# Kernel tuning notes

Hardware: AMD Instinct MI355X
Metric: run time of the kernel (lower is better)

## Reference

```python
import jax, jax.numpy as jnp
import numpy as np

NUM_EXPERTS = 16
TOP_K = 2
D_IN = 1024
D_HID = 4096
D_OUT = 1024
BATCH = 8192


def setup_inputs() -> dict:
    key = jax.random.key(0)
    ks = jax.random.split(key, 6)
    s_in = 1.0 / np.sqrt(D_IN)
    s_hid = 1.0 / np.sqrt(D_HID)
    return {
        "x": jax.random.normal(ks[0], (BATCH, D_IN), dtype=jnp.float32),
        "Wg": jax.random.normal(ks[1], (D_IN, NUM_EXPERTS), dtype=jnp.float32) * s_in,
        "W1": jax.random.normal(ks[2], (NUM_EXPERTS, D_IN, D_HID), dtype=jnp.float32) * s_in,
        "b1": jnp.zeros((NUM_EXPERTS, D_HID), dtype=jnp.float32),
        "W2": jax.random.normal(ks[3], (NUM_EXPERTS, D_HID, D_OUT), dtype=jnp.float32) * s_hid,
        "b2": jnp.zeros((NUM_EXPERTS, D_OUT), dtype=jnp.float32),
    }


def _moe_forward(x, Wg, W1, b1, W2, b2):
    # Gating: top-k routing with softmax over the selected logits.
    logits = x @ Wg                                   # [B, E]
    top_vals, top_idx = jax.lax.top_k(logits, TOP_K)  # [B, k]
    routing_weights = jax.nn.softmax(top_vals, axis=-1)  # [B, k]

    # Per-token combine weight for each expert (sum over k slots):
    # cw[b, e] = sum_k routing_weights[b, k] * (top_idx[b, k] == e)
    one_hot = jax.nn.one_hot(top_idx, NUM_EXPERTS, dtype=x.dtype)  # [B, k, E]
    combine_w = jnp.einsum("bk,bke->be", routing_weights, one_hot)  # [B, E]

    # Per-expert MLP compute + weighted scatter-add combine.
    # Fixed-size loop over experts (structurally distinct weight slices);
    # equivalent math to the original's gather/compute/scatter dispatch.
    out = jnp.zeros((x.shape[0], D_OUT), dtype=x.dtype)
    for e in range(NUM_EXPERTS):
        h = jax.nn.relu(x @ W1[e] + b1[e])            # [B, H]
        y = h @ W2[e] + b2[e]                         # [B, O]
        out = out + combine_w[:, e:e + 1] * y
    return out


def reference(x, Wg, W1, b1, W2, b2):
    return _moe_forward(x, Wg, W1, b1, W2, b2)
```

## Files before the change

kernel.cpp:

```cpp
#include <hip/hip_runtime.h>
#include <cstdio>

#define DIN   1024
#define DHID  4096
#define DOUT  1024
#define NEXP  16
#define NTOK  8192
#define NPAIR (NTOK * 2)
#define PADMAX 20480
#define MAXTILES 80

typedef _Float16 h8 __attribute__((ext_vector_type(8)));
typedef _Float16 h4 __attribute__((ext_vector_type(4)));
typedef float    f4 __attribute__((ext_vector_type(4)));

#define C_CNT  0
#define C_POFF 16
#define C_CUR  32
#define C_NT   48
#define C_TE   64
#define C_TP   256

__device__ __forceinline__ void async16(const void* g, void* l) {
  __builtin_amdgcn_global_load_lds((const __attribute__((address_space(1))) void*)g,
                                   (__attribute__((address_space(3))) void*)l, 16, 0, 0);
}

__global__ void k_init(float* __restrict__ out, const float* __restrict__ x,
                       _Float16* __restrict__ x16, int* __restrict__ ptok,
                       float* __restrict__ pw, int* __restrict__ ctrl) {
  int i = blockIdx.x * 256 + threadIdx.x;
  ((f4*)out)[i] = (f4){0.f, 0.f, 0.f, 0.f};
  float4 v = ((const float4*)x)[i];
  h4 hv = {(_Float16)v.x, (_Float16)v.y, (_Float16)v.z, (_Float16)v.w};
  ((h4*)x16)[i] = hv;
  if (i < PADMAX) { ptok[i] = 0; pw[i] = 0.f; }
  if (i < 1024) ctrl[i] = 0;
}

__global__ void k_gate(const float* __restrict__ x, const float* __restrict__ wg,
                       int* __restrict__ te, float* __restrict__ tw,
                       int* __restrict__ ctrl) {
  int t = blockIdx.x * 4 + (threadIdx.x >> 6);
  int l = threadIdx.x & 63;
  const float* xr = x + (long)t * DIN;
  float acc[NEXP];
#pragma unroll
  for (int e = 0; e < NEXP; ++e) acc[e] = 0.f;
  for (int k = l; k < DIN; k += 64) {
    float xv = xr[k];
    const float4* wr = (const float4*)(wg + (long)k * NEXP);
    float4 a = wr[0], b = wr[1], c = wr[2], d = wr[3];
    acc[0]  += xv * a.x; acc[1]  += xv * a.y; acc[2]  += xv * a.z; acc[3]  += xv * a.w;
    acc[4]  += xv * b.x; acc[5]  += xv * b.y; acc[6]  += xv * b.z; acc[7]  += xv * b.w;
    acc[8]  += xv * c.x; acc[9]  += xv * c.y; acc[10] += xv * c.z; acc[11] += xv * c.w;
    acc[12] += xv * d.x; acc[13] += xv * d.y; acc[14] += xv * d.z; acc[15] += xv * d.w;
  }
#pragma unroll
  for (int off = 32; off > 0; off >>= 1) {
#pragma unroll
    for (int e = 0; e < NEXP; ++e) acc[e] += __shfl_xor(acc[e], off, 64);
  }
  if (l == 0) {
    float v0 = -1e30f; int e0 = 0;
#pragma unroll
    for (int e = 0; e < NEXP; ++e) if (acc[e] > v0) { v0 = acc[e]; e0 = e; }
    float v1 = -1e30f; int e1 = 0;
#pragma unroll
    for (int e = 0; e < NEXP; ++e) if (e != e0 && acc[e] > v1) { v1 = acc[e]; e1 = e; }
    float d = expf(v1 - v0);
    float den = 1.f / (1.f + d);
    te[2 * t] = e0;     tw[2 * t] = den;
    te[2 * t + 1] = e1; tw[2 * t + 1] = d * den;
    atomicAdd(&ctrl[C_CNT + e0], 1);
    atomicAdd(&ctrl[C_CNT + e1], 1);
  }
}

__global__ void k_scan(int* __restrict__ ctrl) {
  __shared__ int sOff[NEXP], sT0[NEXP], sTiles[NEXP];
  int tid = threadIdx.x;
  if (tid == 0) {
    int off = 0, nt = 0;
    for (int e = 0; e < NEXP; ++e) {
      int c = ctrl[C_CNT + e];
      int tiles = (c + 255) >> 8;
      ctrl[C_POFF + e] = off;
      ctrl[C_CUR + e] = off;
      sOff[e] = off; sT0[e] = nt; sTiles[e] = tiles;
      nt += tiles;
      off += tiles * 256;
    }
    ctrl[C_NT] = nt;
  }
  __syncthreads();
  int nt = sT0[NEXP - 1] + sTiles[NEXP - 1];
  for (int j = tid; j < nt; j += blockDim.x) {
    int e = 0;
#pragma unroll
    for (int k = 1; k < NEXP; ++k) if (j >= sT0[k]) e = k;
    ctrl[C_TE + j] = e;
    ctrl[C_TP + j] = sOff[e] + (j - sT0[e]) * 256;
  }
}

__global__ void k_assign(const int* __restrict__ te, const float* __restrict__ tw,
                         int* __restrict__ ctrl, int* __restrict__ ptok,
                         float* __restrict__ pw) {
  int t = blockIdx.x * 256 + threadIdx.x;
#pragma unroll
  for (int s = 0; s < 2; ++s) {
    int e = te[2 * t + s];
    int pos = atomicAdd(&ctrl[C_CUR + e], 1);
    ptok[pos] = t;
    pw[pos] = tw[2 * t + s];
  }
}

__global__ void k_transpose(const float* __restrict__ W, _Float16* __restrict__ out,
                            int R, int C) {
  __shared__ __align__(16) _Float16 lds[64 * 128];
  int e = blockIdx.z;
  const float* Wb = W + ((long)e * R + blockIdx.x * 128) * C + blockIdx.y * 64;
  _Float16* ob = out + ((long)e * C + blockIdx.y * 64) * R + blockIdx.x * 128;
  int tid = threadIdx.x;
  int l = tid & 63, w = tid >> 6;
  int c0 = (l & 15) * 4;
  int rq0 = (l >> 4) * 4 + w * 16;
#pragma unroll
  for (int rr = 0; rr < 2; ++rr) {
    int rq = rq0 + rr * 64;
    float4 v0 = *(const float4*)(Wb + (long)(rq + 0) * C + c0);
    float4 v1 = *(const float4*)(Wb + (long)(rq + 1) * C + c0);
    float4 v2 = *(const float4*)(Wb + (long)(rq + 2) * C + c0);
    float4 v3 = *(const float4*)(Wb + (long)(rq + 3) * C + c0);
    int rchunk = rq >> 3, rsub = rq & 7;
    {
      int c = c0 + 0;
      h4 hv = {(_Float16)v0.x, (_Float16)v1.x, (_Float16)v2.x, (_Float16)v3.x};
      *(h4*)&lds[c * 128 + ((rchunk ^ (c & 15)) << 3) + rsub] = hv;
    }
    {
      int c = c0 + 1;
      h4 hv = {(_Float16)v0.y, (_Float16)v1.y, (_Float16)v2.y, (_Float16)v3.y};
      *(h4*)&lds[c * 128 + ((rchunk ^ (c & 15)) << 3) + rsub] = hv;
    }
    {
      int c = c0 + 2;
      h4 hv = {(_Float16)v0.z, (_Float16)v1.z, (_Float16)v2.z, (_Float16)v3.z};
      *(h4*)&lds[c * 128 + ((rchunk ^ (c & 15)) << 3) + rsub] = hv;
    }
    {
      int c = c0 + 3;
      h4 hv = {(_Float16)v0.w, (_Float16)v1.w, (_Float16)v2.w, (_Float16)v3.w};
      *(h4*)&lds[c * 128 + ((rchunk ^ (c & 15)) << 3) + rsub] = hv;
    }
  }
  __syncthreads();
#pragma unroll
  for (int it = 0; it < 4; ++it) {
    int idx = it * 256 + tid;
    int c = idx >> 4, ch = idx & 15;
    h8 v = *(const h8*)&lds[c * 128 + ((ch ^ (c & 15)) << 3)];
    *(h8*)(ob + (long)c * R + ch * 8) = v;
  }
}

template<int KD, int ND, int G1>
__global__ __launch_bounds__(512, 2)
void k_gemm(const _Float16* __restrict__ A, const _Float16* __restrict__ Wt,
            const float* __restrict__ bias, const int* __restrict__ ctrl,
            const int* __restrict__ ptok, const float* __restrict__ pw,
            _Float16* __restrict__ Hout, float* __restrict__ out) {
  __shared__ __align__(16) _Float16 sm[65536];

  constexpr int NB = ND / 256;
  constexpr int NW = NB * MAXTILES;
  constexpr int QX = NW / 8;
  int bid = blockIdx.x;
  int wid = (bid & 7) * QX + (bid >> 3);
  int nb = wid % NB;
  int mt = wid / NB;

  if (mt >= ctrl[C_NT]) return;
  int e  = ctrl[C_TE + mt];
  int p0 = ctrl[C_TP + mt];
  int n0 = nb * 256;
  int tid = threadIdx.x;
  int w = tid >> 6, l = tid & 63;
  int wm = w & 1, wn = w >> 1;
  int ln15 = l & 15, lq = l >> 4;

  const _Float16* agp[4];
  const _Float16* bgp[4];
#pragma unroll
  for (int h = 0; h < 2; ++h)
#pragma unroll
    for (int j = 0; j < 2; ++j) {
      int r = (w * 2 + j) * 8 + (l >> 3);
      int c = (l & 7) ^ (r & 7);
      long arow = G1 ? (long)ptok[p0 + h * 128 + r] : (long)(p0 + h * 128 + r);
      agp[h * 2 + j] = A + arow * KD + c * 8;
      bgp[h * 2 + j] = Wt + ((long)e * ND + n0 + h * 128 + r) * KD + c * 8;
    }

  auto stageH = [&](int t, int half) {
    _Float16* dst = sm + (t & 1) * 32768 + (half & 1) * 16384 + (half >> 1) * 8192
                    + w * 1024;
    long koff = (long)t * 64;
    const _Float16* const* gp = (half & 1) ? bgp : agp;
#pragma unroll
    for (int j = 0; j < 2; ++j)
      async16(gp[(half >> 1) * 2 + j] + koff, dst + j * 512);
  };

  f4 acc[2][4][2][2];
#pragma unroll
  for (int mq = 0; mq < 2; ++mq)
#pragma unroll
    for (int i = 0; i < 4; ++i)
#pragma unroll
      for (int nq = 0; nq < 2; ++nq)
#pragma unroll
        for (int j = 0; j < 2; ++j) acc[mq][i][nq][j] = (f4){0.f, 0.f, 0.f, 0.f};

  h8 af[8], bf0[4], bf1[4];

  auto readA = [&](int d, int mq) {
    const _Float16* Ab = sm + d * 32768 + mq * 8192;
#pragma unroll
    for (int i = 0; i < 4; ++i) {
      int rh = wm * 64 + i * 16 + ln15;
#pragma unroll
      for (int ks = 0; ks < 2; ++ks)
        af[i * 2 + ks] = *(const h8*)&Ab[rh * 64 + (((ks * 4 + lq)) ^ (rh & 7)) * 8];
    }
  };
  auto readB = [&](int d, int nq, h8* bf) {
    const _Float16* Bb = sm + d * 32768 + 16384 + nq * 8192;
#pragma unroll
    for (int j = 0; j < 2; ++j) {
      int rh = wn * 32 + j * 16 + ln15;
#pragma unroll
      for (int ks = 0; ks < 2; ++ks)
        bf[j * 2 + ks] = *(const h8*)&Bb[rh * 64 + (((ks * 4 + lq)) ^ (rh & 7)) * 8];
    }
  };
  auto mfmaQ = [&](int mq, int nq, const h8* bf) {
    __builtin_amdgcn_s_setprio(1);
#pragma unroll
    for (int ks = 0; ks < 2; ++ks)
#pragma unroll
      for (int i = 0; i < 4; ++i)
#pragma unroll
        for (int j = 0; j < 2; ++j)
          acc[mq][i][nq][j] = __builtin_amdgcn_mfma_f32_16x16x32_f16(
              af[i * 2 + ks], bf[j * 2 + ks], acc[mq][i][nq][j], 0, 0, 0);
    __builtin_amdgcn_s_setprio(0);
  };

  constexpr int KSTEPS = KD / 64;

  stageH(0, 0); stageH(0, 1); stageH(0, 2); stageH(0, 3);
  stageH(1, 0); stageH(1, 1); stageH(1, 2);
  asm volatile("s_waitcnt vmcnt(6)" ::: "memory");
  __builtin_amdgcn_s_barrier();

#pragma unroll 2
  for (int t = 0; t < KSTEPS; ++t) {
    int d = t & 1;
    readA(d, 0);
    readB(d, 0, bf0);
    if (t + 1 < KSTEPS) stageH(t + 1, 3);
    __builtin_amdgcn_s_barrier();
    asm volatile("s_waitcnt lgkmcnt(0)" ::: "memory");
    mfmaQ(0, 0, bf0);
    __builtin_amdgcn_s_barrier();
    readB(d, 1, bf1);
    if (t + 2 < KSTEPS) stageH(t + 2, 0);
    __builtin_amdgcn_s_barrier();
    asm volatile("s_waitcnt lgkmcnt(0)" ::: "memory");
    mfmaQ(0, 1, bf1);
    __builtin_amdgcn_s_barrier();
    readA(d, 1);
    if (t + 2 < KSTEPS) stageH(t + 2, 1);
    __builtin_amdgcn_s_barrier();
    asm volatile("s_waitcnt lgkmcnt(0)" ::: "memory");
    mfmaQ(1, 1, bf1);
    __builtin_amdgcn_s_barrier();
    if (t + 2 < KSTEPS) stageH(t + 2, 2);
    if (t + 1 < KSTEPS) {
      if (t + 2 < KSTEPS) asm volatile("s_waitcnt vmcnt(6)" ::: "memory");
      else                asm volatile("s_waitcnt vmcnt(0)" ::: "memory");
    }
    __builtin_amdgcn_s_barrier();
    mfmaQ(1, 0, bf0);
    __builtin_amdgcn_s_barrier();
  }

  float bj[2][2];
#pragma unroll
  for (int nq = 0; nq < 2; ++nq)
#pragma unroll
    for (int j = 0; j < 2; ++j)
      bj[nq][j] = bias[e * ND + n0 + nq * 128 + wn * 32 + j * 16 + ln15];

  if (G1) {
    _Float16* cs = sm;
#pragma unroll
    for (int mq = 0; mq < 2; ++mq) {
      if (mq) __syncthreads();
#pragma unroll
      for (int i = 0; i < 4; ++i)
#pragma unroll
        for (int reg = 0; reg < 4; ++reg) {
          int row = wm * 64 + i * 16 + lq * 4 + reg;
#pragma unroll
          for (int nq = 0; nq < 2; ++nq)
#pragma unroll
            for (int j = 0; j < 2; ++j)
              cs[row * 264 + nq * 128 + wn * 32 + j * 16 + ln15] =
                  (_Float16)fmaxf(acc[mq][i][nq][j][reg] + bj[nq][j], 0.f);
        }
      __syncthreads();
#pragma unroll
      for (int p = 0; p < 8; ++p) {
        int idx = p * 512 + tid;
        int row = idx >> 5, ch = idx & 31;
        *(h8*)(Hout + (long)(p0 + mq * 128 + row) * DHID + n0 + ch * 8) =
            *(const h8*)&cs[row * 264 + ch * 8];
      }
    }
  } else {
#pragma unroll
    for (int mq = 0; mq < 2; ++mq)
#pragma unroll
      for (int i = 0; i < 4; ++i)
#pragma unroll
        for (int reg = 0; reg < 4; ++reg) {
          int p = p0 + mq * 128 + wm * 64 + i * 16 + lq * 4 + reg;
          float wgt = pw[p];
          if (wgt != 0.f) {
            int tk = ptok[p];
            float* orow = out + (long)tk * DOUT + n0;
#pragma unroll
            for (int nq = 0; nq < 2; ++nq)
#pragma unroll
              for (int j = 0; j < 2; ++j)
                atomicAdd(&orow[nq * 128 + wn * 32 + j * 16 + ln15],
                          wgt * (acc[mq][i][nq][j][reg] + bj[nq][j]));
          }
        }
  }
}

extern "C" void kernel_launch(void* const* d_in, const int* in_sizes, int n_in,
                              void* d_out, int out_size, void* d_ws, size_t ws_size,
                              hipStream_t stream) {
  const float* x  = (const float*)d_in[0];
  const float* Wg = (const float*)d_in[1];
  const float* W1 = (const float*)d_in[2];
  const float* b1 = (const float*)d_in[3];
  const float* W2 = (const float*)d_in[4];
  const float* b2 = (const float*)d_in[5];
  float* out = (float*)d_out;
  char* ws = (char*)d_ws;

  size_t WT_OFF = 0;
  size_t H_OFF  = WT_OFF + (size_t)NEXP * DHID * DIN * 2;
  size_t X_OFF  = H_OFF  + (size_t)PADMAX * DHID * 2;
  size_t TE_OFF = X_OFF  + (size_t)NTOK * DIN * 2;
  size_t TW_OFF = TE_OFF + (size_t)NPAIR * 4;
  size_t PT_OFF = TW_OFF + (size_t)NPAIR * 4;
  size_t PW_OFF = PT_OFF + (size_t)PADMAX * 4;
  size_t CT_OFF = PW_OFF + (size_t)PADMAX * 4;
  size_t END    = CT_OFF + 4096;
  if (ws_size < END) {
    fprintf(stderr, "kernel_launch: ws too small (%zu < %zu)\n", ws_size, END);
    return;
  }
  _Float16* Wt  = (_Float16*)(ws + WT_OFF);
  _Float16* H   = (_Float16*)(ws + H_OFF);
  _Float16* x16 = (_Float16*)(ws + X_OFF);
  int*   te   = (int*)(ws + TE_OFF);
  float* tw   = (float*)(ws + TW_OFF);
  int*   pt   = (int*)(ws + PT_OFF);
  float* pw   = (float*)(ws + PW_OFF);
  int*   ctrl = (int*)(ws + CT_OFF);

  k_init<<<NTOK * DIN / (256 * 4), 256, 0, stream>>>(out, x, x16, pt, pw, ctrl);
  k_gate<<<NTOK / 4, 256, 0, stream>>>(x, Wg, te, tw, ctrl);
  k_scan<<<1, 256, 0, stream>>>(ctrl);
  k_assign<<<NTOK / 256, 256, 0, stream>>>(te, tw, ctrl, pt, pw);

  k_transpose<<<dim3(DIN / 128, DHID / 64, NEXP), 256, 0, stream>>>(W1, Wt, DIN, DHID);
  k_gemm<DIN, DHID, 1><<<dim3((DHID / 256) * MAXTILES), 512, 0, stream>>>(
      x16, Wt, b1, ctrl, pt, pw, H, nullptr);

  k_transpose<<<dim3(DHID / 128, DOUT / 64, NEXP), 256, 0, stream>>>(W2, Wt, DHID, DOUT);
  k_gemm<DHID, DOUT, 0><<<dim3((DOUT / 256) * MAXTILES), 512, 0, stream>>>(
      H, Wt, b2, ctrl, pt, pw, nullptr, out);
}
```

Before: 1.266 ms.

## Simplify GEMM main loop to single-stage prefetch and rewrite weight transpose

The GEMM main loop loses its finely interleaved schedule of quarter-tile staging, split barriers and partial vmcnt waits. Instead it issues all four staging loads for the next k-step up front, reads both A halves and both B halves into registers, runs all MFMAs, then waits for all loads and issues one barrier per step. The weight transpose kernel also becomes a simpler 64x64 padded fp32 LDS tile that converts to fp16 on readback. Holding a second A fragment set raises register pressure, and the coarser overlap may hide global-load latency less well than the old staggered pipeline.

```diff
diff --git a/kernel.cpp b/kernel.cpp
--- a/kernel.cpp
+++ b/kernel.cpp
@@ -119,50 +119,35 @@
 
 __global__ void k_transpose(const float* __restrict__ W, _Float16* __restrict__ out,
                             int R, int C) {
-  __shared__ __align__(16) _Float16 lds[64 * 128];
+  __shared__ float tileT[64][65];
   int e = blockIdx.z;
-  const float* Wb = W + ((long)e * R + blockIdx.x * 128) * C + blockIdx.y * 64;
-  _Float16* ob = out + ((long)e * C + blockIdx.y * 64) * R + blockIdx.x * 128;
-  int tid = threadIdx.x;
-  int l = tid & 63, w = tid >> 6;
-  int c0 = (l & 15) * 4;
-  int rq0 = (l >> 4) * 4 + w * 16;
-#pragma unroll
-  for (int rr = 0; rr < 2; ++rr) {
-    int rq = rq0 + rr * 64;
-    float4 v0 = *(const float4*)(Wb + (long)(rq + 0) * C + c0);
-    float4 v1 = *(const float4*)(Wb + (long)(rq + 1) * C + c0);
-    float4 v2 = *(const float4*)(Wb + (long)(rq + 2) * C + c0);
-    float4 v3 = *(const float4*)(Wb + (long)(rq + 3) * C + c0);
-    int rchunk = rq >> 3, rsub = rq & 7;
-    {
-      int c = c0 + 0;
-      h4 hv = {(_Float16)v0.x, (_Float16)v1.x, (_Float16)v2.x, (_Float16)v3.x};
-      *(h4*)&lds[c * 128 + ((rchunk ^ (c & 15)) << 3) + rsub] = hv;
-    }
-    {
-      int c = c0 + 1;
-      h4 hv = {(_Float16)v0.y, (_Float16)v1.y, (_Float16)v2.y, (_Float16)v3.y};
-      *(h4*)&lds[c * 128 + ((rchunk ^ (c & 15)) << 3) + rsub] = hv;
-    }
-    {
-      int c = c0 + 2;
-      h4 hv = {(_Float16)v0.z, (_Float16)v1.z, (_Float16)v2.z, (_Float16)v3.z};
-      *(h4*)&lds[c * 128 + ((rchunk ^ (c & 15)) << 3) + rsub] = hv;
-    }
-    {
-      int c = c0 + 3;
-      h4 hv = {(_Float16)v0.w, (_Float16)v1.w, (_Float16)v2.w, (_Float16)v3.w};
-      *(h4*)&lds[c * 128 + ((rchunk ^ (c & 15)) << 3) + rsub] = hv;
-    }
+  const float* Wb = W + ((long)e * R + blockIdx.x * 64) * C + blockIdx.y * 64;
+  _Float16* ob = out + ((long)e * C + blockIdx.y * 64) * R + blockIdx.x * 64;
+  int t = threadIdx.x;
+  int r0 = t >> 4;
+  int c4 = (t & 15) * 4;
+#pragma unroll
+  for (int i = 0; i < 4; ++i) {
+    int r = r0 + i * 16;
+    float4 v = *(const float4*)(Wb + (long)r * C + c4);
+    tileT[c4 + 0][r] = v.x;
+    tileT[c4 + 1][r] = v.y;
+    tileT[c4 + 2][r] = v.z;
+    tileT[c4 + 3][r] = v.w;
   }
   __syncthreads();
-#pragma unroll
-  for (int it = 0; it < 4; ++it) {
-    int idx = it * 256 + tid;
-    int c = idx >> 4, ch = idx & 15;
-    h8 v = *(const h8*)&lds[c * 128 + ((ch ^ (c & 15)) << 3)];
-    *(h8*)(ob + (long)c * R + ch * 8) = v;
+  int c = t >> 2;
+  int rb = (t & 3) * 16;
+  float f[16];
+#pragma unroll
+  for (int k = 0; k < 16; ++k) f[k] = tileT[c][rb + k];
+#pragma unroll
+  for (int k = 0; k < 2; ++k) {
+    h8 hv = {(_Float16)f[k * 8 + 0], (_Float16)f[k * 8 + 1],
+             (_Float16)f[k * 8 + 2], (_Float16)f[k * 8 + 3],
+             (_Float16)f[k * 8 + 4], (_Float16)f[k * 8 + 5],
+             (_Float16)f[k * 8 + 6], (_Float16)f[k * 8 + 7]};
+    *(h8*)(ob + (long)c * R + rb + k * 8) = hv;
   }
 }
 
@@ -224,16 +209,16 @@
 #pragma unroll
         for (int j = 0; j < 2; ++j) acc[mq][i][nq][j] = (f4){0.f, 0.f, 0.f, 0.f};
 
-  h8 af[8], bf0[4], bf1[4];
-
-  auto readA = [&](int d, int mq) {
+  h8 af[8], af2[8], bf0[4], bf1[4];
+
+  auto readA = [&](int d, int mq, h8* dst) {
     const _Float16* Ab = sm + d * 32768 + mq * 8192;
 #pragma unroll
     for (int i = 0; i < 4; ++i) {
       int rh = wm * 64 + i * 16 + ln15;
 #pragma unroll
       for (int ks = 0; ks < 2; ++ks)
-        af[i * 2 + ks] = *(const h8*)&Ab[rh * 64 + (((ks * 4 + lq)) ^ (rh & 7)) * 8];
+        dst[i * 2 + ks] = *(const h8*)&Ab[rh * 64 + (((ks * 4 + lq)) ^ (rh & 7)) * 8];
     }
   };
   auto readB = [&](int d, int nq, h8* bf) {
@@ -246,7 +231,7 @@
         bf[j * 2 + ks] = *(const h8*)&Bb[rh * 64 + (((ks * 4 + lq)) ^ (rh & 7)) * 8];
     }
   };
-  auto mfmaQ = [&](int mq, int nq, const h8* bf) {
+  auto mfmaQ = [&](int mq, int nq, const h8* a, const h8* bf) {
     __builtin_amdgcn_s_setprio(1);
 #pragma unroll
     for (int ks = 0; ks < 2; ++ks)
@@ -255,46 +240,31 @@
 #pragma unroll
         for (int j = 0; j < 2; ++j)
           acc[mq][i][nq][j] = __builtin_amdgcn_mfma_f32_16x16x32_f16(
-              af[i * 2 + ks], bf[j * 2 + ks], acc[mq][i][nq][j], 0, 0, 0);
+              a[i * 2 + ks], bf[j * 2 + ks], acc[mq][i][nq][j], 0, 0, 0);
     __builtin_amdgcn_s_setprio(0);
   };
 
   constexpr int KSTEPS = KD / 64;
 
   stageH(0, 0); stageH(0, 1); stageH(0, 2); stageH(0, 3);
-  stageH(1, 0); stageH(1, 1); stageH(1, 2);
-  asm volatile("s_waitcnt vmcnt(6)" ::: "memory");
+  asm volatile("s_waitcnt vmcnt(0)" ::: "memory");
   __builtin_amdgcn_s_barrier();
 
 #pragma unroll 2
   for (int t = 0; t < KSTEPS; ++t) {
     int d = t & 1;
-    readA(d, 0);
+    if (t + 1 < KSTEPS) {
+      stageH(t + 1, 0); stageH(t + 1, 1); stageH(t + 1, 2); stageH(t + 1, 3);
+    }
+    readA(d, 0, af);
     readB(d, 0, bf0);
-    if (t + 1 < KSTEPS) stageH(t + 1, 3);
-    __builtin_amdgcn_s_barrier();
-    asm volatile("s_waitcnt lgkmcnt(0)" ::: "memory");
-    mfmaQ(0, 0, bf0);
-    __builtin_amdgcn_s_barrier();
     readB(d, 1, bf1);
-    if (t + 2 < KSTEPS) stageH(t + 2, 0);
-    __builtin_amdgcn_s_barrier();
-    asm volatile("s_waitcnt lgkmcnt(0)" ::: "memory");
-    mfmaQ(0, 1, bf1);
-    __builtin_amdgcn_s_barrier();
-    readA(d, 1);
-    if (t + 2 < KSTEPS) stageH(t + 2, 1);
-    __builtin_amdgcn_s_barrier();
-    asm volatile("s_waitcnt lgkmcnt(0)" ::: "memory");
-    mfmaQ(1, 1, bf1);
-    __builtin_amdgcn_s_barrier();
-    if (t + 2 < KSTEPS) stageH(t + 2, 2);
-    if (t + 1 < KSTEPS) {
-      if (t + 2 < KSTEPS) asm volatile("s_waitcnt vmcnt(6)" ::: "memory");
-      else                asm volatile("s_waitcnt vmcnt(0)" ::: "memory");
-    }
-    __builtin_amdgcn_s_barrier();
-    mfmaQ(1, 0, bf0);
+    readA(d, 1, af2);
+    mfmaQ(0, 0, af,  bf0);
+    mfmaQ(0, 1, af,  bf1);
+    mfmaQ(1, 1, af2, bf1);
+    mfmaQ(1, 0, af2, bf0);
+    if (t + 1 < KSTEPS) asm volatile("s_waitcnt vmcnt(0)" ::: "memory");
     __builtin_amdgcn_s_barrier();
   }
 
@@ -393,11 +363,11 @@
   k_scan<<<1, 256, 0, stream>>>(ctrl);
   k_assign<<<NTOK / 256, 256, 0, stream>>>(te, tw, ctrl, pt, pw);
 
-  k_transpose<<<dim3(DIN / 128, DHID / 64, NEXP), 256, 0, stream>>>(W1, Wt, DIN, DHID);
+  k_transpose<<<dim3(DIN / 64, DHID / 64, NEXP), 256, 0, stream>>>(W1, Wt, DIN, DHID);
   k_gemm<DIN, DHID, 1><<<dim3((DHID / 256) * MAXTILES), 512, 0, stream>>>(
       x16, Wt, b1, ctrl, pt, pw, H, nullptr);
 
-  k_transpose<<<dim3(DHID / 128, DOUT / 64, NEXP), 256, 0, stream>>>(W2, Wt, DHID, DOUT);
+  k_transpose<<<dim3(DHID / 64, DOUT / 64, NEXP), 256, 0, stream>>>(W2, Wt, DHID, DOUT);
   k_gemm<DHID, DOUT, 0><<<dim3((DOUT / 256) * MAXTILES), 512, 0, stream>>>(
       H, Wt, b2, ctrl, pt, pw, nullptr, out);
 }
```

New measurement: 1.847 ms. 46.0% more time.
